# Optimization experiments

Hardware: AMD Instinct MI355X
Metric: run time of the kernel (lower is better)

## Reference

```python
import jax, jax.numpy as jnp
import numpy as np

N_NODES = 1_000_000
N_EDGES = 16_000_000


def setup_inputs() -> dict:
    key = jax.random.key(0)
    k1, k2, k3, k4 = jax.random.split(key, 4)
    x = jax.random.normal(k1, (N_NODES, 2), dtype=jnp.float32)
    edge_index = jax.random.randint(k2, (2, N_EDGES), 0, N_NODES, dtype=jnp.int64)
    W1 = jax.random.normal(k3, (2, 4), dtype=jnp.float32) * 0.5
    b1 = jnp.zeros((4,), dtype=jnp.float32)
    W2 = jax.random.normal(k4, (4, 2), dtype=jnp.float32) * 0.5
    b2 = jnp.zeros((2,), dtype=jnp.float32)
    return {"x": x, "edge_index": edge_index, "W1": W1, "b1": b1, "W2": W2, "b2": b2}


def _gcn_conv(h, src, dst, norm, b, n_nodes):
    # h already linearly transformed: message = h[src] * norm, scatter-add to dst
    msg = h[src] * norm[:, None]
    out = jax.ops.segment_sum(msg, dst, num_segments=n_nodes)
    return out + b


def reference(x, edge_index, W1, b1, W2, b2):
    n = x.shape[0]
    loop = jnp.arange(n, dtype=edge_index.dtype)
    # PyG GCNConv default: add self-loops, symmetric deg^{-1/2} normalization
    src = jnp.concatenate([edge_index[0], loop])
    dst = jnp.concatenate([edge_index[1], loop])
    deg = jax.ops.segment_sum(jnp.ones_like(src, dtype=x.dtype), dst, num_segments=n)
    dinv = jnp.where(deg > 0, jax.lax.rsqrt(deg), 0.0)
    norm = dinv[src] * dinv[dst]

    h = _gcn_conv(x @ W1, src, dst, norm, b1, n)   # conv1: [N,2] -> [N,4]
    h = jax.nn.relu(h)
    out = _gcn_conv(h @ W2, src, dst, norm, b2, n)  # conv2: [N,4] -> [N,2]
    return out
```

## Files before the change

kernel.cpp:

```cpp
#include <hip/hip_runtime.h>
#include <hip/hip_fp16.h>


constexpr int W_SHIFT = 11;
constexpr int W = 2048;
constexpr int MAXB = 512;
constexpr int RB = 1024;
constexpr int CHUNK = 8192;
constexpr int CAP = 28;
constexpr int AB = 512;

constexpr float SCALE1 = 65536.0f;
constexpr float INV1   = 1.0f / 65536.0f;
constexpr unsigned BIAS1 = 1u << 20;
constexpr float SCALE2 = 4096.0f;
constexpr float INV2   = 1.0f / 4096.0f;
constexpr unsigned BIAS2 = 1u << 22;

typedef unsigned uv4 __attribute__((ext_vector_type(4)));
typedef int      iv4 __attribute__((ext_vector_type(4)));

__device__ __forceinline__ unsigned long long pack2(float a, float b,
                                                    float scale, unsigned bias) {
    unsigned lo = (unsigned)(__float2int_rn(a * scale) + (int)bias);
    unsigned hi = (unsigned)(__float2int_rn(b * scale) + (int)bias);
    return (unsigned long long)lo | ((unsigned long long)hi << 32);
}

__global__ __launch_bounds__(256) void k_zero_fill(unsigned* __restrict__ fill,
                                                   int nb, unsigned C) {
    int i = blockIdx.x * 256 + threadIdx.x;
    if (i < nb) fill[i] = (unsigned)i * C;
}

__global__ __launch_bounds__(RB) void k_reorder(const int* __restrict__ src,
                                                const int* __restrict__ dst,
                                                unsigned* __restrict__ fill,
                                                unsigned* __restrict__ perm, int E) {
    __shared__ unsigned slab[MAXB * CAP];
    __shared__ unsigned ptr[MAXB];
    __shared__ unsigned gbase[MAXB];
    int tid = threadIdx.x;
    if (tid < MAXB) ptr[tid] = 0u;
    __syncthreads();
    long base0 = (long)blockIdx.x * CHUNK;
    int total = (int)min((long)CHUNK, (long)E - base0);
    bool full = (total == CHUNK);

    if (full) {
        const iv4* dv4 = (const iv4*)(dst + base0);
        const iv4* sv4 = (const iv4*)(src + base0);
        #pragma unroll
        for (int k = 0; k < 2; k++) {
            iv4 dq = dv4[k * RB + tid];
            iv4 sq = sv4[k * RB + tid];
            unsigned d, b, val, lpos;
            d = (unsigned)dq.x; b = d >> W_SHIFT;
            val = (unsigned)sq.x | ((d & (W - 1)) << 20);
            lpos = atomicAdd(&ptr[b], 1u);
            if (lpos < (unsigned)CAP) slab[b * CAP + lpos] = val;
            else perm[atomicAdd(&fill[b], 1u)] = val;
            d = (unsigned)dq.y; b = d >> W_SHIFT;
            val = (unsigned)sq.y | ((d & (W - 1)) << 20);
            lpos = atomicAdd(&ptr[b], 1u);
            if (lpos < (unsigned)CAP) slab[b * CAP + lpos] = val;
            else perm[atomicAdd(&fill[b], 1u)] = val;
            d = (unsigned)dq.z; b = d >> W_SHIFT;
            val = (unsigned)sq.z | ((d & (W - 1)) << 20);
            lpos = atomicAdd(&ptr[b], 1u);
            if (lpos < (unsigned)CAP) slab[b * CAP + lpos] = val;
            else perm[atomicAdd(&fill[b], 1u)] = val;
            d = (unsigned)dq.w; b = d >> W_SHIFT;
            val = (unsigned)sq.w | ((d & (W - 1)) << 20);
            lpos = atomicAdd(&ptr[b], 1u);
            if (lpos < (unsigned)CAP) slab[b * CAP + lpos] = val;
            else perm[atomicAdd(&fill[b], 1u)] = val;
        }
    } else {
        for (int li = tid; li < total; li += RB) {
            unsigned d = (unsigned)dst[base0 + li];
            unsigned s = (unsigned)src[base0 + li];
            unsigned b = d >> W_SHIFT;
            unsigned val = s | ((d & (W - 1)) << 20);
            unsigned lpos = atomicAdd(&ptr[b], 1u);
            if (lpos < (unsigned)CAP) slab[b * CAP + lpos] = val;
            else perm[atomicAdd(&fill[b], 1u)] = val;
        }
    }
    __syncthreads();
    if (tid < MAXB) {
        unsigned cnt = min(ptr[tid], (unsigned)CAP);
        gbase[tid] = cnt ? atomicAdd(&fill[tid], cnt) : 0u;
        ptr[tid] = cnt;
    }
    __syncthreads();
    for (int s = tid; s < MAXB * CAP; s += RB) {
        int b = s / CAP;
        int i = s - b * CAP;
        if (i < (int)ptr[b]) perm[gbase[b] + i] = slab[s];
    }
}

__global__ __launch_bounds__(AB) void k_dinv(const unsigned* __restrict__ perm,
                                             const unsigned* __restrict__ fill,
                                             const float2* __restrict__ x,
                                             float* __restrict__ dinv,
                                             unsigned* __restrict__ deg,
                                             __half2* __restrict__ xs,
                                             int N, unsigned C) {
    __shared__ unsigned c[2 * W];
    for (int i = threadIdx.x; i < 2 * W; i += AB) c[i] = 0u;
    __syncthreads();
    int b = blockIdx.x;
    unsigned par = threadIdx.x & 1u;
    unsigned s = (unsigned)b * C, e = fill[b];
    unsigned m = e - s, nv8 = m >> 3;
    const uv4* p4 = (const uv4*)(perm + s);
    for (unsigned j = threadIdx.x; j < nv8; j += AB) {
        uv4 qa = __builtin_nontemporal_load(p4 + 2u * j);
        uv4 qb = __builtin_nontemporal_load(p4 + 2u * j + 1u);
        atomicAdd(&c[((qa.x >> 20) << 1) | par], 1u);
        atomicAdd(&c[((qa.y >> 20) << 1) | par], 1u);
        atomicAdd(&c[((qa.z >> 20) << 1) | par], 1u);
        atomicAdd(&c[((qa.w >> 20) << 1) | par], 1u);
        atomicAdd(&c[((qb.x >> 20) << 1) | par], 1u);
        atomicAdd(&c[((qb.y >> 20) << 1) | par], 1u);
        atomicAdd(&c[((qb.z >> 20) << 1) | par], 1u);
        atomicAdd(&c[((qb.w >> 20) << 1) | par], 1u);
    }
    unsigned t = s + (nv8 << 3) + threadIdx.x;
    if (t < e) atomicAdd(&c[((perm[t] >> 20) << 1) | par], 1u);
    __syncthreads();
    int d0 = b << W_SHIFT;
    for (int l = threadIdx.x; l < W; l += AB) {
        int d = d0 + l;
        if (d < N) {
            unsigned cn = c[2 * l] + c[2 * l + 1];
            float dv = 1.0f / sqrtf((float)(cn + 1u));
            dinv[d] = dv;
            deg[d] = cn;
            float2 xv = x[d];
            xs[d] = __floats2half2_rn(xv.x * dv, xv.y * dv);
        }
    }
}

__global__ __launch_bounds__(AB) void k_acc1(const unsigned* __restrict__ perm,
                                             const unsigned* __restrict__ fill,
                                             const __half2* __restrict__ xs,
                                             const float* __restrict__ dinv,
                                             const unsigned* __restrict__ deg,
                                             const float* __restrict__ W1,
                                             const float* __restrict__ b1,
                                             const float* __restrict__ W2,
                                             __half2* __restrict__ h2s,
                                             int N, unsigned C) {
    __shared__ unsigned long long acc[2 * W];
    for (int i = threadIdx.x; i < 2 * W; i += AB) acc[i] = 0ull;
    __syncthreads();
    int b = blockIdx.x;
    unsigned par = threadIdx.x & 1u;
    unsigned s = (unsigned)b * C, e = fill[b];
    unsigned m = e - s, nv8 = m >> 3;
    const uv4* p4 = (const uv4*)(perm + s);
    for (unsigned j = threadIdx.x; j < nv8; j += AB) {
        uv4 qa = __builtin_nontemporal_load(p4 + 2u * j);
        uv4 qb = __builtin_nontemporal_load(p4 + 2u * j + 1u);
        float2 v0 = __half22float2(xs[qa.x & 0xFFFFFu]);
        float2 v1 = __half22float2(xs[qa.y & 0xFFFFFu]);
        float2 v2 = __half22float2(xs[qa.z & 0xFFFFFu]);
        float2 v3 = __half22float2(xs[qa.w & 0xFFFFFu]);
        float2 v4 = __half22float2(xs[qb.x & 0xFFFFFu]);
        float2 v5 = __half22float2(xs[qb.y & 0xFFFFFu]);
        float2 v6 = __half22float2(xs[qb.z & 0xFFFFFu]);
        float2 v7 = __half22float2(xs[qb.w & 0xFFFFFu]);
        atomicAdd(&acc[((qa.x >> 20) << 1) | par], pack2(v0.x, v0.y, SCALE1, BIAS1));
        atomicAdd(&acc[((qa.y >> 20) << 1) | par], pack2(v1.x, v1.y, SCALE1, BIAS1));
        atomicAdd(&acc[((qa.z >> 20) << 1) | par], pack2(v2.x, v2.y, SCALE1, BIAS1));
        atomicAdd(&acc[((qa.w >> 20) << 1) | par], pack2(v3.x, v3.y, SCALE1, BIAS1));
        atomicAdd(&acc[((qb.x >> 20) << 1) | par], pack2(v4.x, v4.y, SCALE1, BIAS1));
        atomicAdd(&acc[((qb.y >> 20) << 1) | par], pack2(v5.x, v5.y, SCALE1, BIAS1));
        atomicAdd(&acc[((qb.z >> 20) << 1) | par], pack2(v6.x, v6.y, SCALE1, BIAS1));
        atomicAdd(&acc[((qb.w >> 20) << 1) | par], pack2(v7.x, v7.y, SCALE1, BIAS1));
    }
    unsigned t = s + (nv8 << 3) + threadIdx.x;
    if (t < e) {
        unsigned p = perm[t];
        float2 v = __half22float2(xs[p & 0xFFFFFu]);
        atomicAdd(&acc[((p >> 20) << 1) | par], pack2(v.x, v.y, SCALE1, BIAS1));
    }
    __syncthreads();
    int d0 = b << W_SHIFT;
    float w10 = W1[0], w11 = W1[1], w12 = W1[2], w13 = W1[3];
    float w14 = W1[4], w15 = W1[5], w16 = W1[6], w17 = W1[7];
    float bb0 = b1[0], bb1 = b1[1], bb2 = b1[2], bb3 = b1[3];
    float u0 = W2[0], u1 = W2[1], u2 = W2[2], u3 = W2[3];
    float u4 = W2[4], u5 = W2[5], u6 = W2[6], u7 = W2[7];
    for (int l = threadIdx.x; l < W; l += AB) {
        int d = d0 + l;
        if (d < N) {
            float dv = dinv[d];
            unsigned cn = deg[d];
            unsigned long long a64 = acc[2 * l] + acc[2 * l + 1];
            unsigned lo = (unsigned)a64, hi = (unsigned)(a64 >> 32);
            float2 self = __half22float2(xs[d]);
            float Sx = (float)(int)(lo - cn * BIAS1) * INV1 + self.x;
            float Sy = (float)(int)(hi - cn * BIAS1) * INV1 + self.y;
            float a0 = fmaxf(fmaf(Sy, w14, Sx * w10) * dv + bb0, 0.0f);
            float a1 = fmaxf(fmaf(Sy, w15, Sx * w11) * dv + bb1, 0.0f);
            float a2 = fmaxf(fmaf(Sy, w16, Sx * w12) * dv + bb2, 0.0f);
            float a3 = fmaxf(fmaf(Sy, w17, Sx * w13) * dv + bb3, 0.0f);
            float hx = (a0 * u0 + a1 * u2 + a2 * u4 + a3 * u6) * dv;
            float hy = (a0 * u1 + a1 * u3 + a2 * u5 + a3 * u7) * dv;
            h2s[d] = __floats2half2_rn(hx, hy);
        }
    }
}

__global__ __launch_bounds__(AB) void k_acc2(const unsigned* __restrict__ perm,
                                             const unsigned* __restrict__ fill,
                                             const __half2* __restrict__ h2s,
                                             const float* __restrict__ dinv,
                                             const unsigned* __restrict__ deg,
                                             const float* __restrict__ b2,
                                             float2* __restrict__ out,
                                             int N, unsigned C) {
    __shared__ unsigned long long acc[2 * W];
    for (int i = threadIdx.x; i < 2 * W; i += AB) acc[i] = 0ull;
    __syncthreads();
    int b = blockIdx.x;
    unsigned par = threadIdx.x & 1u;
    unsigned s = (unsigned)b * C, e = fill[b];
    unsigned m = e - s, nv8 = m >> 3;
    const uv4* p4 = (const uv4*)(perm + s);
    for (unsigned j = threadIdx.x; j < nv8; j += AB) {
        uv4 qa = __builtin_nontemporal_load(p4 + 2u * j);
        uv4 qb = __builtin_nontemporal_load(p4 + 2u * j + 1u);
        float2 v0 = __half22float2(h2s[qa.x & 0xFFFFFu]);
        float2 v1 = __half22float2(h2s[qa.y & 0xFFFFFu]);
        float2 v2 = __half22float2(h2s[qa.z & 0xFFFFFu]);
        float2 v3 = __half22float2(h2s[qa.w & 0xFFFFFu]);
        float2 v4 = __half22float2(h2s[qb.x & 0xFFFFFu]);
        float2 v5 = __half22float2(h2s[qb.y & 0xFFFFFu]);
        float2 v6 = __half22float2(h2s[qb.z & 0xFFFFFu]);
        float2 v7 = __half22float2(h2s[qb.w & 0xFFFFFu]);
        atomicAdd(&acc[((qa.x >> 20) << 1) | par], pack2(v0.x, v0.y, SCALE2, BIAS2));
        atomicAdd(&acc[((qa.y >> 20) << 1) | par], pack2(v1.x, v1.y, SCALE2, BIAS2));
        atomicAdd(&acc[((qa.z >> 20) << 1) | par], pack2(v2.x, v2.y, SCALE2, BIAS2));
        atomicAdd(&acc[((qa.w >> 20) << 1) | par], pack2(v3.x, v3.y, SCALE2, BIAS2));
        atomicAdd(&acc[((qb.x >> 20) << 1) | par], pack2(v4.x, v4.y, SCALE2, BIAS2));
        atomicAdd(&acc[((qb.y >> 20) << 1) | par], pack2(v5.x, v5.y, SCALE2, BIAS2));
        atomicAdd(&acc[((qb.z >> 20) << 1) | par], pack2(v6.x, v6.y, SCALE2, BIAS2));
        atomicAdd(&acc[((qb.w >> 20) << 1) | par], pack2(v7.x, v7.y, SCALE2, BIAS2));
    }
    unsigned t = s + (nv8 << 3) + threadIdx.x;
    if (t < e) {
        unsigned p = perm[t];
        float2 v = __half22float2(h2s[p & 0xFFFFFu]);
        atomicAdd(&acc[((p >> 20) << 1) | par], pack2(v.x, v.y, SCALE2, BIAS2));
    }
    __syncthreads();
    int d0 = b << W_SHIFT;
    float bb0 = b2[0], bb1 = b2[1];
    for (int l = threadIdx.x; l < W; l += AB) {
        int d = d0 + l;
        if (d < N) {
            float dv = dinv[d];
            unsigned cn = deg[d];
            unsigned long long a64 = acc[2 * l] + acc[2 * l + 1];
            unsigned lo = (unsigned)a64, hi = (unsigned)(a64 >> 32);
            float2 v = __half22float2(h2s[d]);
            float Sx = (float)(int)(lo - cn * BIAS2) * INV2 + v.x;
            float Sy = (float)(int)(hi - cn * BIAS2) * INV2 + v.y;
            out[d] = make_float2(Sx * dv + bb0, Sy * dv + bb1);
        }
    }
}


__global__ __launch_bounds__(256) void f_init_deg(unsigned* deg, int n) {
    int i = blockIdx.x * 256 + threadIdx.x;
    if (i < n) deg[i] = 1u;
}
__global__ __launch_bounds__(256) void f_count_deg(const int* dst, unsigned* deg, int E) {
    int e = blockIdx.x * 256 + threadIdx.x;
    if (e < E) atomicAdd(&deg[dst[e]], 1u);
}
__global__ __launch_bounds__(256) void f_node1(const float2* x, const float* W1,
                                               const unsigned* deg, float* dinv,
                                               float4* h1s, float4* agg1, int n) {
    int i = blockIdx.x * 256 + threadIdx.x;
    if (i >= n) return;
    float dv = 1.0f / sqrtf((float)deg[i]);
    dinv[i] = dv;
    float2 xv = x[i];
    float4 h;
    h.x = fmaf(xv.y, W1[4], xv.x * W1[0]) * dv;
    h.y = fmaf(xv.y, W1[5], xv.x * W1[1]) * dv;
    h.z = fmaf(xv.y, W1[6], xv.x * W1[2]) * dv;
    h.w = fmaf(xv.y, W1[7], xv.x * W1[3]) * dv;
    h1s[i] = h;
    agg1[i] = make_float4(h.x * dv, h.y * dv, h.z * dv, h.w * dv);
}
__global__ __launch_bounds__(256) void f_edge1(const int* src, const int* dst,
                                               const float* dinv, const float4* h1s,
                                               float* agg1, int E) {
    int e = blockIdx.x * 256 + threadIdx.x;
    if (e >= E) return;
    int s = src[e], d = dst[e];
    float w = dinv[d];
    float4 m = h1s[s];
    float* p = agg1 + 4ll * d;
    unsafeAtomicAdd(p + 0, m.x * w);
    unsafeAtomicAdd(p + 1, m.y * w);
    unsafeAtomicAdd(p + 2, m.z * w);
    unsafeAtomicAdd(p + 3, m.w * w);
}
__global__ __launch_bounds__(256) void f_node2(const float4* agg1, const float* b1,
                                               const float* W2, const float* b2,
                                               const float* dinv, float2* h2s,
                                               float2* out, int n) {
    int i = blockIdx.x * 256 + threadIdx.x;
    if (i >= n) return;
    float4 a = agg1[i];
    a.x = fmaxf(a.x + b1[0], 0.0f);
    a.y = fmaxf(a.y + b1[1], 0.0f);
    a.z = fmaxf(a.z + b1[2], 0.0f);
    a.w = fmaxf(a.w + b1[3], 0.0f);
    float dv = dinv[i];
    float2 h;
    h.x = (a.x * W2[0] + a.y * W2[2] + a.z * W2[4] + a.w * W2[6]) * dv;
    h.y = (a.x * W2[1] + a.y * W2[3] + a.z * W2[5] + a.w * W2[7]) * dv;
    h2s[i] = h;
    out[i] = make_float2(b2[0] + h.x * dv, b2[1] + h.y * dv);
}
__global__ __launch_bounds__(256) void f_edge2(const int* src, const int* dst,
                                               const float* dinv, const float2* h2s,
                                               float* out, int E) {
    int e = blockIdx.x * 256 + threadIdx.x;
    if (e >= E) return;
    int s = src[e], d = dst[e];
    float w = dinv[d];
    float2 m = h2s[s];
    float* p = out + 2ll * d;
    unsafeAtomicAdd(p + 0, m.x * w);
    unsafeAtomicAdd(p + 1, m.y * w);
}

extern "C" void kernel_launch(void* const* d_in, const int* in_sizes, int n_in,
                              void* d_out, int out_size, void* d_ws, size_t ws_size,
                              hipStream_t stream) {
    const float* x  = (const float*)d_in[0];
    const int* ei   = (const int*)d_in[1];
    const float* W1 = (const float*)d_in[2];
    const float* b1 = (const float*)d_in[3];
    const float* W2 = (const float*)d_in[4];
    const float* b2 = (const float*)d_in[5];
    float* out = (float*)d_out;

    const int N = in_sizes[0] / 2;
    const int E = in_sizes[1] / 2;
    const int* src = ei;
    const int* dst = ei + E;
    const int NB = (N + W - 1) >> W_SHIFT;

    char* ws = (char*)d_ws;
    const int gN = (N + 255) / 256;
    const int gE = (E + 255) / 256;

    size_t fixed = 32768 + (size_t)16 * N;
    long avail = (long)ws_size - (long)fixed;
    long Cmax = (avail > 0) ? avail / (4L * NB) : 0;
    long Cmin = (long)(E / (NB > 0 ? NB : 1)) + 4096;
    long Cw = (Cmax > Cmin + 8192) ? (Cmin + 8192) : Cmax;
    unsigned C = (unsigned)(Cw & ~7L);
    bool fast = ((long)C >= Cmin) && (NB <= MAXB) && (N <= (1 << 20));

    if (fast) {
        unsigned* fill = (unsigned*)(ws);
        float*    dinv = (float*)(ws + 32768);
        unsigned* deg  = (unsigned*)(ws + 32768 + (size_t)4 * N);
        __half2*  xs   = (__half2*)(ws + 32768 + (size_t)8 * N);
        __half2*  h2s  = (__half2*)(ws + 32768 + (size_t)12 * N);
        unsigned* perm = (unsigned*)(ws + fixed);

        k_zero_fill<<<(NB + 255) / 256, 256, 0, stream>>>(fill, NB, C);
        k_reorder<<<(E + CHUNK - 1) / CHUNK, RB, 0, stream>>>(src, dst, fill, perm, E);
        k_dinv<<<NB, AB, 0, stream>>>(perm, fill, (const float2*)x, dinv, deg, xs, N, C);
        k_acc1<<<NB, AB, 0, stream>>>(perm, fill, xs, dinv, deg, W1, b1, W2, h2s, N, C);
        k_acc2<<<NB, AB, 0, stream>>>(perm, fill, h2s, dinv, deg, b2, (float2*)out, N, C);
    } else {
        unsigned* deg = (unsigned*)(ws);
        float* dinv   = (float*)(ws + (size_t)4 * N);
        float* h1s    = (float*)(ws + (size_t)8 * N);
        float* agg1   = (float*)(ws + (size_t)24 * N);
        float* h2s    = h1s;

        f_init_deg<<<gN, 256, 0, stream>>>(deg, N);
        f_count_deg<<<gE, 256, 0, stream>>>(dst, deg, E);
        f_node1<<<gN, 256, 0, stream>>>((const float2*)x, W1, deg, dinv,
                                        (float4*)h1s, (float4*)agg1, N);
        f_edge1<<<gE, 256, 0, stream>>>(src, dst, dinv, (const float4*)h1s, agg1, E);
        f_node2<<<gN, 256, 0, stream>>>((const float4*)agg1, b1, W2, b2, dinv,
                                        (float2*)h2s, (float2*)out, N);
        f_edge2<<<gE, 256, 0, stream>>>(src, dst, dinv, (const float2*)h2s, out, E);
    }
}
```

Measured before the change: 431.3 us.

## Build per-destination CSR within windows and use gather-based accumulation

Adds a second-level sort that turns each destination window's bucketed edges into a full CSR (offsets plus source list). Degrees and dinv are computed from the counts in the same pass. The two aggregation passes become pull-style gathers per destination node with register accumulation, replacing the shared-memory atomic scatter over each window. The cost is an extra read and write of the edge list plus more workspace, and the per-thread loops can be imbalanced when degrees vary.

```diff
diff --git a/kernel.cpp b/kernel.cpp
--- a/kernel.cpp
+++ b/kernel.cpp
@@ -101,6 +101,205 @@
     }
 }
 
+__global__ __launch_bounds__(AB) void k_sortwin(const unsigned* __restrict__ perm,
+                                                const unsigned* __restrict__ fill,
+                                                const float2* __restrict__ x,
+                                                __half2* __restrict__ xs,
+                                                unsigned* __restrict__ offs,
+                                                unsigned* __restrict__ perm2,
+                                                int N, unsigned C, int NB) {
+    __shared__ unsigned cnt[2 * W];
+    __shared__ unsigned scn[AB];
+    __shared__ unsigned sh_base, sh_tot;
+    const int tid = threadIdx.x;
+    const int b = blockIdx.x;
+
+    unsigned wsz = (tid < NB) ? (fill[tid] - (unsigned)tid * C) : 0u;
+    scn[tid] = wsz;
+    __syncthreads();
+    for (int off = 1; off < AB; off <<= 1) {
+        unsigned u = (tid >= off) ? scn[tid - off] : 0u;
+        __syncthreads();
+        scn[tid] += u;
+        __syncthreads();
+    }
+    if (tid == 0) {
+        sh_base = (b > 0) ? scn[b - 1] : 0u;
+        sh_tot  = scn[AB - 1];
+    }
+    for (int i = tid; i < 2 * W; i += AB) cnt[i] = 0u;
+    __syncthreads();
+
+    unsigned s = (unsigned)b * C, e = fill[b];
+    unsigned m = e - s, nv8 = m >> 3;
+    unsigned par = tid & 1u;
+    const uv4* p4 = (const uv4*)(perm + s);
+    for (unsigned j = tid; j < nv8; j += AB) {
+        uv4 qa = __builtin_nontemporal_load(p4 + 2u * j);
+        uv4 qb = __builtin_nontemporal_load(p4 + 2u * j + 1u);
+        atomicAdd(&cnt[((qa.x >> 20) << 1) | par], 1u);
+        atomicAdd(&cnt[((qa.y >> 20) << 1) | par], 1u);
+        atomicAdd(&cnt[((qa.z >> 20) << 1) | par], 1u);
+        atomicAdd(&cnt[((qa.w >> 20) << 1) | par], 1u);
+        atomicAdd(&cnt[((qb.x >> 20) << 1) | par], 1u);
+        atomicAdd(&cnt[((qb.y >> 20) << 1) | par], 1u);
+        atomicAdd(&cnt[((qb.z >> 20) << 1) | par], 1u);
+        atomicAdd(&cnt[((qb.w >> 20) << 1) | par], 1u);
+    }
+    unsigned t8 = s + (nv8 << 3) + (unsigned)tid;
+    if (t8 < e) atomicAdd(&cnt[((perm[t8] >> 20) << 1) | par], 1u);
+    __syncthreads();
+
+    int l0 = 4 * tid;
+    unsigned c0 = cnt[2 * l0]     + cnt[2 * l0 + 1];
+    unsigned c1 = cnt[2 * l0 + 2] + cnt[2 * l0 + 3];
+    unsigned c2 = cnt[2 * l0 + 4] + cnt[2 * l0 + 5];
+    unsigned c3 = cnt[2 * l0 + 6] + cnt[2 * l0 + 7];
+    unsigned sum4 = c0 + c1 + c2 + c3;
+    scn[tid] = sum4;
+    __syncthreads();
+    for (int off = 1; off < AB; off <<= 1) {
+        unsigned u = (tid >= off) ? scn[tid - off] : 0u;
+        __syncthreads();
+        scn[tid] += u;
+        __syncthreads();
+    }
+    unsigned base = sh_base + (scn[tid] - sum4);
+    unsigned o0 = base, o1 = o0 + c0, o2 = o1 + c1, o3 = o2 + c2;
+    cnt[l0] = o0; cnt[l0 + 1] = o1; cnt[l0 + 2] = o2; cnt[l0 + 3] = o3;
+
+    int d0 = (b << W_SHIFT) + l0;
+    if (d0     <= N) offs[d0]     = o0;
+    if (d0 + 1 <= N) offs[d0 + 1] = o1;
+    if (d0 + 2 <= N) offs[d0 + 2] = o2;
+    if (d0 + 3 <= N) offs[d0 + 3] = o3;
+    if (b == 0 && tid == 0) offs[N] = sh_tot;
+
+    unsigned cc[4] = {c0, c1, c2, c3};
+    #pragma unroll
+    for (int k = 0; k < 4; k++) {
+        int d = d0 + k;
+        if (d < N) {
+            float dv = 1.0f / sqrtf((float)cc[k] + 1.0f);
+            float2 xv = x[d];
+            xs[d] = __floats2half2_rn(xv.x * dv, xv.y * dv);
+        }
+    }
+    __syncthreads();
+
+    for (unsigned j = tid; j < nv8; j += AB) {
+        uv4 qa = __builtin_nontemporal_load(p4 + 2u * j);
+        uv4 qb = __builtin_nontemporal_load(p4 + 2u * j + 1u);
+        unsigned p;
+        p = atomicAdd(&cnt[qa.x >> 20], 1u); perm2[p] = qa.x & 0xFFFFFu;
+        p = atomicAdd(&cnt[qa.y >> 20], 1u); perm2[p] = qa.y & 0xFFFFFu;
+        p = atomicAdd(&cnt[qa.z >> 20], 1u); perm2[p] = qa.z & 0xFFFFFu;
+        p = atomicAdd(&cnt[qa.w >> 20], 1u); perm2[p] = qa.w & 0xFFFFFu;
+        p = atomicAdd(&cnt[qb.x >> 20], 1u); perm2[p] = qb.x & 0xFFFFFu;
+        p = atomicAdd(&cnt[qb.y >> 20], 1u); perm2[p] = qb.y & 0xFFFFFu;
+        p = atomicAdd(&cnt[qb.z >> 20], 1u); perm2[p] = qb.z & 0xFFFFFu;
+        p = atomicAdd(&cnt[qb.w >> 20], 1u); perm2[p] = qb.w & 0xFFFFFu;
+    }
+    if (t8 < e) {
+        unsigned v = perm[t8];
+        unsigned p = atomicAdd(&cnt[v >> 20], 1u);
+        perm2[p] = v & 0xFFFFFu;
+    }
+}
+
+__global__ __launch_bounds__(AB) void k_gacc1(const unsigned* __restrict__ perm2,
+                                              const unsigned* __restrict__ offs,
+                                              const __half2* __restrict__ xs,
+                                              const float* __restrict__ W1,
+                                              const float* __restrict__ b1,
+                                              const float* __restrict__ W2,
+                                              __half2* __restrict__ h2s, int N) {
+    int d0 = (blockIdx.x << W_SHIFT) + 4 * (int)threadIdx.x;
+    if (d0 >= N) return;
+    uv4 ov = *(const uv4*)(offs + d0);
+    unsigned o4 = offs[d0 + 4];
+    float w10 = W1[0], w11 = W1[1], w12 = W1[2], w13 = W1[3];
+    float w14 = W1[4], w15 = W1[5], w16 = W1[6], w17 = W1[7];
+    float bb0 = b1[0], bb1 = b1[1], bb2 = b1[2], bb3 = b1[3];
+    float u0 = W2[0], u1 = W2[1], u2 = W2[2], u3 = W2[3];
+    float u4 = W2[4], u5 = W2[5], u6 = W2[6], u7 = W2[7];
+    unsigned stA[4] = {ov.x, ov.y, ov.z, ov.w};
+    unsigned enA[4] = {ov.y, ov.z, ov.w, o4};
+    #pragma unroll
+    for (int k = 0; k < 4; k++) {
+        int d = d0 + k;
+        if (d < N) {
+            unsigned st = stA[k], en = enA[k];
+            float dv = 1.0f / sqrtf((float)(en - st) + 1.0f);
+            float2 self = __half22float2(xs[d]);
+            float Sx = self.x, Sy = self.y;
+            unsigned i = st;
+            for (; i + 4 <= en; i += 4) {
+                unsigned s0 = perm2[i], s1 = perm2[i + 1];
+                unsigned s2 = perm2[i + 2], s3 = perm2[i + 3];
+                float2 v0 = __half22float2(xs[s0]);
+                float2 v1 = __half22float2(xs[s1]);
+                float2 v2 = __half22float2(xs[s2]);
+                float2 v3 = __half22float2(xs[s3]);
+                Sx += (v0.x + v1.x) + (v2.x + v3.x);
+                Sy += (v0.y + v1.y) + (v2.y + v3.y);
+            }
+            for (; i < en; i++) {
+                float2 v = __half22float2(xs[perm2[i]]);
+                Sx += v.x; Sy += v.y;
+            }
+            float a0 = fmaxf(fmaf(Sy, w14, Sx * w10) * dv + bb0, 0.0f);
+            float a1 = fmaxf(fmaf(Sy, w15, Sx * w11) * dv + bb1, 0.0f);
+            float a2 = fmaxf(fmaf(Sy, w16, Sx * w12) * dv + bb2, 0.0f);
+            float a3 = fmaxf(fmaf(Sy, w17, Sx * w13) * dv + bb3, 0.0f);
+            float hx = (a0 * u0 + a1 * u2 + a2 * u4 + a3 * u6) * dv;
+            float hy = (a0 * u1 + a1 * u3 + a2 * u5 + a3 * u7) * dv;
+            h2s[d] = __floats2half2_rn(hx, hy);
+        }
+    }
+}
+
+__global__ __launch_bounds__(AB) void k_gacc2(const unsigned* __restrict__ perm2,
+                                              const unsigned* __restrict__ offs,
+                                              const __half2* __restrict__ h2s,
+                                              const float* __restrict__ b2,
+                                              float2* __restrict__ out, int N) {
+    int d0 = (blockIdx.x << W_SHIFT) + 4 * (int)threadIdx.x;
+    if (d0 >= N) return;
+    uv4 ov = *(const uv4*)(offs + d0);
+    unsigned o4 = offs[d0 + 4];
+    float bb0 = b2[0], bb1 = b2[1];
+    unsigned stA[4] = {ov.x, ov.y, ov.z, ov.w};
+    unsigned enA[4] = {ov.y, ov.z, ov.w, o4};
+    #pragma unroll
+    for (int k = 0; k < 4; k++) {
+        int d = d0 + k;
+        if (d < N) {
+            unsigned st = stA[k], en = enA[k];
+            float dv = 1.0f / sqrtf((float)(en - st) + 1.0f);
+            float2 self = __half22float2(h2s[d]);
+            float Sx = self.x, Sy = self.y;
+            unsigned i = st;
+            for (; i + 4 <= en; i += 4) {
+                unsigned s0 = perm2[i], s1 = perm2[i + 1];
+                unsigned s2 = perm2[i + 2], s3 = perm2[i + 3];
+                float2 v0 = __half22float2(h2s[s0]);
+                float2 v1 = __half22float2(h2s[s1]);
+                float2 v2 = __half22float2(h2s[s2]);
+                float2 v3 = __half22float2(h2s[s3]);
+                Sx += (v0.x + v1.x) + (v2.x + v3.x);
+                Sy += (v0.y + v1.y) + (v2.y + v3.y);
+            }
+            for (; i < en; i++) {
+                float2 v = __half22float2(h2s[perm2[i]]);
+                Sx += v.x; Sy += v.y;
+            }
+            out[d] = make_float2(Sx * dv + bb0, Sy * dv + bb1);
+        }
+    }
+}
+
+
 __global__ __launch_bounds__(AB) void k_dinv(const unsigned* __restrict__ perm,
                                              const unsigned* __restrict__ fill,
                                              const float2* __restrict__ x,
@@ -368,15 +567,41 @@
     const int gN = (N + 255) / 256;
     const int gE = (E + 255) / 256;
 
+    const long Cmin = (long)(E / (NB > 0 ? NB : 1)) + 4096;
+    auto rnd = [](size_t v) { return (v + 63) & ~(size_t)63; };
+
+    size_t sz_xs   = rnd((size_t)4 * N);
+    size_t sz_offs = rnd((size_t)4 * (N + 16));
+    size_t sz_p2   = rnd((size_t)4 * (size_t)E);
+    size_t fixed2  = 32768 + sz_xs + sz_xs + sz_offs + sz_p2 + 64;
+    long avail2 = (long)ws_size - (long)fixed2;
+    long Cmax2 = (avail2 > 0) ? avail2 / (4L * NB) : 0;
+    long Cw2 = (Cmax2 > Cmin + 8192) ? (Cmin + 8192) : Cmax2;
+    unsigned C2 = (unsigned)(Cw2 & ~7L);
+    bool fast2 = ((long)C2 >= Cmin) && (NB <= MAXB) && (N <= (1 << 20)) && (E > 0);
+
     size_t fixed = 32768 + (size_t)16 * N;
     long avail = (long)ws_size - (long)fixed;
     long Cmax = (avail > 0) ? avail / (4L * NB) : 0;
-    long Cmin = (long)(E / (NB > 0 ? NB : 1)) + 4096;
     long Cw = (Cmax > Cmin + 8192) ? (Cmin + 8192) : Cmax;
     unsigned C = (unsigned)(Cw & ~7L);
     bool fast = ((long)C >= Cmin) && (NB <= MAXB) && (N <= (1 << 20));
 
-    if (fast) {
+    if (fast2) {
+        unsigned* fill  = (unsigned*)ws;
+        __half2*  xs    = (__half2*)(ws + 32768);
+        __half2*  h2s   = (__half2*)(ws + 32768 + sz_xs);
+        unsigned* offs  = (unsigned*)(ws + 32768 + 2 * sz_xs);
+        unsigned* perm2 = (unsigned*)(ws + 32768 + 2 * sz_xs + sz_offs);
+        unsigned* perm  = (unsigned*)(ws + 32768 + 2 * sz_xs + sz_offs + sz_p2);
+
+        k_zero_fill<<<(NB + 255) / 256, 256, 0, stream>>>(fill, NB, C2);
+        k_reorder<<<(E + CHUNK - 1) / CHUNK, RB, 0, stream>>>(src, dst, fill, perm, E);
+        k_sortwin<<<NB, AB, 0, stream>>>(perm, fill, (const float2*)x, xs, offs,
+                                         perm2, N, C2, NB);
+        k_gacc1<<<NB, AB, 0, stream>>>(perm2, offs, xs, W1, b1, W2, h2s, N);
+        k_gacc2<<<NB, AB, 0, stream>>>(perm2, offs, h2s, b2, (float2*)out, N);
+    } else if (fast) {
         unsigned* fill = (unsigned*)(ws);
         float*    dinv = (float*)(ws + 32768);
         unsigned* deg  = (unsigned*)(ws + 32768 + (size_t)4 * N);
```

New measurement: 810.4 us. 87.9% more time.

## Fuse reorder, degree and both aggregation stages into one cooperative kernel

Applied to the files above, without the earlier changes.

Replaces the five separate launches (fill init, edge reorder, degree/dinv, conv1, conv2) with a single cooperative kernel. Stages are separated by grid-wide syncs, and one shared-memory union holds the slab, count and accumulator buffers. The reorder stage becomes a grid-stride loop over chunks run by NB blocks of 512 threads. The goal is to remove per-launch gaps and the separate dinv buffer. The cost is far fewer resident waves during the reorder stage, plus grid-sync overhead.

```diff
diff --git a/kernel.cpp b/kernel.cpp
--- a/kernel.cpp
+++ b/kernel.cpp
@@ -1,5 +1,8 @@
 #include <hip/hip_runtime.h>
 #include <hip/hip_fp16.h>
+#include <hip/hip_cooperative_groups.h>
+
+namespace cg = cooperative_groups;
 
 
 constexpr int W_SHIFT = 11;
@@ -8,6 +11,7 @@
 constexpr int RB = 1024;
 constexpr int CHUNK = 8192;
 constexpr int CAP = 28;
+constexpr int CT = 512;
 constexpr int AB = 512;
 
 constexpr float SCALE1 = 65536.0f;
@@ -26,6 +30,246 @@
     unsigned hi = (unsigned)(__float2int_rn(b * scale) + (int)bias);
     return (unsigned long long)lo | ((unsigned long long)hi << 32);
 }
+
+
+__global__ __launch_bounds__(CT, 4) void k_fused(
+    const int* __restrict__ src, const int* __restrict__ dst,
+    const float2* __restrict__ x,
+    const float* __restrict__ W1, const float* __restrict__ b1,
+    const float* __restrict__ W2, const float* __restrict__ b2,
+    unsigned* __restrict__ fill, unsigned* __restrict__ deg,
+    __half2* __restrict__ xs, __half2* __restrict__ h2s,
+    float2* __restrict__ out, unsigned* __restrict__ perm,
+    int N, int E, unsigned C, int NB, int NCH)
+{
+    __shared__ union ShU {
+        struct { unsigned slab[MAXB * CAP]; unsigned ptr[MAXB]; unsigned gbase[MAXB]; } r;
+        unsigned cnt[2 * W];
+        unsigned long long acc[2 * W];
+    } sh;
+    cg::grid_group grid = cg::this_grid();
+    const int tid = threadIdx.x;
+    const int bid = blockIdx.x;
+    const int b = bid;
+
+    if (bid == 0 && tid < NB) fill[tid] = (unsigned)tid * C;
+    grid.sync();
+
+    for (int cid = bid; cid < NCH; cid += gridDim.x) {
+        if (tid < MAXB) sh.r.ptr[tid] = 0u;
+        __syncthreads();
+        long base0 = (long)cid * CHUNK;
+        int total = (int)min((long)CHUNK, (long)E - base0);
+        bool full = (total == CHUNK);
+        if (full) {
+            const iv4* dv4 = (const iv4*)(dst + base0);
+            const iv4* sv4 = (const iv4*)(src + base0);
+            #pragma unroll
+            for (int k = 0; k < CHUNK / (4 * CT); k++) {
+                iv4 dq = dv4[k * CT + tid];
+                iv4 sq = sv4[k * CT + tid];
+                unsigned d, bb, val, lpos;
+                d = (unsigned)dq.x; bb = d >> W_SHIFT;
+                val = (unsigned)sq.x | ((d & (W - 1)) << 20);
+                lpos = atomicAdd(&sh.r.ptr[bb], 1u);
+                if (lpos < (unsigned)CAP) sh.r.slab[bb * CAP + lpos] = val;
+                else perm[atomicAdd(&fill[bb], 1u)] = val;
+                d = (unsigned)dq.y; bb = d >> W_SHIFT;
+                val = (unsigned)sq.y | ((d & (W - 1)) << 20);
+                lpos = atomicAdd(&sh.r.ptr[bb], 1u);
+                if (lpos < (unsigned)CAP) sh.r.slab[bb * CAP + lpos] = val;
+                else perm[atomicAdd(&fill[bb], 1u)] = val;
+                d = (unsigned)dq.z; bb = d >> W_SHIFT;
+                val = (unsigned)sq.z | ((d & (W - 1)) << 20);
+                lpos = atomicAdd(&sh.r.ptr[bb], 1u);
+                if (lpos < (unsigned)CAP) sh.r.slab[bb * CAP + lpos] = val;
+                else perm[atomicAdd(&fill[bb], 1u)] = val;
+                d = (unsigned)dq.w; bb = d >> W_SHIFT;
+                val = (unsigned)sq.w | ((d & (W - 1)) << 20);
+                lpos = atomicAdd(&sh.r.ptr[bb], 1u);
+                if (lpos < (unsigned)CAP) sh.r.slab[bb * CAP + lpos] = val;
+                else perm[atomicAdd(&fill[bb], 1u)] = val;
+            }
+        } else {
+            for (int li = tid; li < total; li += CT) {
+                unsigned d = (unsigned)dst[base0 + li];
+                unsigned s = (unsigned)src[base0 + li];
+                unsigned bb = d >> W_SHIFT;
+                unsigned val = s | ((d & (W - 1)) << 20);
+                unsigned lpos = atomicAdd(&sh.r.ptr[bb], 1u);
+                if (lpos < (unsigned)CAP) sh.r.slab[bb * CAP + lpos] = val;
+                else perm[atomicAdd(&fill[bb], 1u)] = val;
+            }
+        }
+        __syncthreads();
+        if (tid < MAXB) {
+            unsigned cnt = min(sh.r.ptr[tid], (unsigned)CAP);
+            sh.r.gbase[tid] = cnt ? atomicAdd(&fill[tid], cnt) : 0u;
+            sh.r.ptr[tid] = cnt;
+        }
+        __syncthreads();
+        for (int s2 = tid; s2 < MAXB * CAP; s2 += CT) {
+            int b2 = s2 / CAP;
+            int i2 = s2 - b2 * CAP;
+            if (i2 < (int)sh.r.ptr[b2]) perm[sh.r.gbase[b2] + i2] = sh.r.slab[s2];
+        }
+        __syncthreads();
+    }
+    __threadfence();
+    grid.sync();
+
+    {
+        for (int i = tid; i < 2 * W; i += CT) sh.cnt[i] = 0u;
+        __syncthreads();
+        unsigned par = tid & 1u;
+        unsigned s = (unsigned)b * C, e = fill[b];
+        unsigned m = e - s, nv8 = m >> 3;
+        const uv4* p4 = (const uv4*)(perm + s);
+        for (unsigned j = tid; j < nv8; j += CT) {
+            uv4 qa = __builtin_nontemporal_load(p4 + 2u * j);
+            uv4 qb = __builtin_nontemporal_load(p4 + 2u * j + 1u);
+            atomicAdd(&sh.cnt[((qa.x >> 20) << 1) | par], 1u);
+            atomicAdd(&sh.cnt[((qa.y >> 20) << 1) | par], 1u);
+            atomicAdd(&sh.cnt[((qa.z >> 20) << 1) | par], 1u);
+            atomicAdd(&sh.cnt[((qa.w >> 20) << 1) | par], 1u);
+            atomicAdd(&sh.cnt[((qb.x >> 20) << 1) | par], 1u);
+            atomicAdd(&sh.cnt[((qb.y >> 20) << 1) | par], 1u);
+            atomicAdd(&sh.cnt[((qb.z >> 20) << 1) | par], 1u);
+            atomicAdd(&sh.cnt[((qb.w >> 20) << 1) | par], 1u);
+        }
+        unsigned t = s + (nv8 << 3) + (unsigned)tid;
+        if (t < e) atomicAdd(&sh.cnt[((perm[t] >> 20) << 1) | par], 1u);
+        __syncthreads();
+        int d0 = b << W_SHIFT;
+        for (int l = tid; l < W; l += CT) {
+            int d = d0 + l;
+            if (d < N) {
+                unsigned cn = sh.cnt[2 * l] + sh.cnt[2 * l + 1];
+                float dv = 1.0f / sqrtf((float)(cn + 1u));
+                deg[d] = cn;
+                float2 xv = x[d];
+                xs[d] = __floats2half2_rn(xv.x * dv, xv.y * dv);
+            }
+        }
+    }
+    __threadfence();
+    grid.sync();
+
+    {
+        for (int i = tid; i < 2 * W; i += CT) sh.acc[i] = 0ull;
+        __syncthreads();
+        unsigned par = tid & 1u;
+        unsigned s = (unsigned)b * C, e = fill[b];
+        unsigned m = e - s, nv8 = m >> 3;
+        const uv4* p4 = (const uv4*)(perm + s);
+        for (unsigned j = tid; j < nv8; j += CT) {
+            uv4 qa = __builtin_nontemporal_load(p4 + 2u * j);
+            uv4 qb = __builtin_nontemporal_load(p4 + 2u * j + 1u);
+            float2 v0 = __half22float2(xs[qa.x & 0xFFFFFu]);
+            float2 v1 = __half22float2(xs[qa.y & 0xFFFFFu]);
+            float2 v2 = __half22float2(xs[qa.z & 0xFFFFFu]);
+            float2 v3 = __half22float2(xs[qa.w & 0xFFFFFu]);
+            float2 v4 = __half22float2(xs[qb.x & 0xFFFFFu]);
+            float2 v5 = __half22float2(xs[qb.y & 0xFFFFFu]);
+            float2 v6 = __half22float2(xs[qb.z & 0xFFFFFu]);
+            float2 v7 = __half22float2(xs[qb.w & 0xFFFFFu]);
+            atomicAdd(&sh.acc[((qa.x >> 20) << 1) | par], pack2(v0.x, v0.y, SCALE1, BIAS1));
+            atomicAdd(&sh.acc[((qa.y >> 20) << 1) | par], pack2(v1.x, v1.y, SCALE1, BIAS1));
+            atomicAdd(&sh.acc[((qa.z >> 20) << 1) | par], pack2(v2.x, v2.y, SCALE1, BIAS1));
+            atomicAdd(&sh.acc[((qa.w >> 20) << 1) | par], pack2(v3.x, v3.y, SCALE1, BIAS1));
+            atomicAdd(&sh.acc[((qb.x >> 20) << 1) | par], pack2(v4.x, v4.y, SCALE1, BIAS1));
+            atomicAdd(&sh.acc[((qb.y >> 20) << 1) | par], pack2(v5.x, v5.y, SCALE1, BIAS1));
+            atomicAdd(&sh.acc[((qb.z >> 20) << 1) | par], pack2(v6.x, v6.y, SCALE1, BIAS1));
+            atomicAdd(&sh.acc[((qb.w >> 20) << 1) | par], pack2(v7.x, v7.y, SCALE1, BIAS1));
+        }
+        unsigned t = s + (nv8 << 3) + (unsigned)tid;
+        if (t < e) {
+            unsigned p = perm[t];
+            float2 v = __half22float2(xs[p & 0xFFFFFu]);
+            atomicAdd(&sh.acc[((p >> 20) << 1) | par], pack2(v.x, v.y, SCALE1, BIAS1));
+        }
+        __syncthreads();
+        int d0 = b << W_SHIFT;
+        float w10 = W1[0], w11 = W1[1], w12 = W1[2], w13 = W1[3];
+        float w14 = W1[4], w15 = W1[5], w16 = W1[6], w17 = W1[7];
+        float bb0 = b1[0], bb1 = b1[1], bb2 = b1[2], bb3 = b1[3];
+        float u0 = W2[0], u1 = W2[1], u2 = W2[2], u3 = W2[3];
+        float u4 = W2[4], u5 = W2[5], u6 = W2[6], u7 = W2[7];
+        for (int l = tid; l < W; l += CT) {
+            int d = d0 + l;
+            if (d < N) {
+                unsigned cn = deg[d];
+                float dv = 1.0f / sqrtf((float)(cn + 1u));
+                unsigned long long a64 = sh.acc[2 * l] + sh.acc[2 * l + 1];
+                unsigned lo = (unsigned)a64, hi = (unsigned)(a64 >> 32);
+                float2 self = __half22float2(xs[d]);
+                float Sx = (float)(int)(lo - cn * BIAS1) * INV1 + self.x;
+                float Sy = (float)(int)(hi - cn * BIAS1) * INV1 + self.y;
+                float a0 = fmaxf(fmaf(Sy, w14, Sx * w10) * dv + bb0, 0.0f);
+                float a1 = fmaxf(fmaf(Sy, w15, Sx * w11) * dv + bb1, 0.0f);
+                float a2 = fmaxf(fmaf(Sy, w16, Sx * w12) * dv + bb2, 0.0f);
+                float a3 = fmaxf(fmaf(Sy, w17, Sx * w13) * dv + bb3, 0.0f);
+                float hx = (a0 * u0 + a1 * u2 + a2 * u4 + a3 * u6) * dv;
+                float hy = (a0 * u1 + a1 * u3 + a2 * u5 + a3 * u7) * dv;
+                h2s[d] = __floats2half2_rn(hx, hy);
+            }
+        }
+    }
+    __threadfence();
+    grid.sync();
+
+    {
+        for (int i = tid; i < 2 * W; i += CT) sh.acc[i] = 0ull;
+        __syncthreads();
+        unsigned par = tid & 1u;
+        unsigned s = (unsigned)b * C, e = fill[b];
+        unsigned m = e - s, nv8 = m >> 3;
+        const uv4* p4 = (const uv4*)(perm + s);
+        for (unsigned j = tid; j < nv8; j += CT) {
+            uv4 qa = __builtin_nontemporal_load(p4 + 2u * j);
+            uv4 qb = __builtin_nontemporal_load(p4 + 2u * j + 1u);
+            float2 v0 = __half22float2(h2s[qa.x & 0xFFFFFu]);
+            float2 v1 = __half22float2(h2s[qa.y & 0xFFFFFu]);
+            float2 v2 = __half22float2(h2s[qa.z & 0xFFFFFu]);
+            float2 v3 = __half22float2(h2s[qa.w & 0xFFFFFu]);
+            float2 v4 = __half22float2(h2s[qb.x & 0xFFFFFu]);
+            float2 v5 = __half22float2(h2s[qb.y & 0xFFFFFu]);
+            float2 v6 = __half22float2(h2s[qb.z & 0xFFFFFu]);
+            float2 v7 = __half22float2(h2s[qb.w & 0xFFFFFu]);
+            atomicAdd(&sh.acc[((qa.x >> 20) << 1) | par], pack2(v0.x, v0.y, SCALE2, BIAS2));
+            atomicAdd(&sh.acc[((qa.y >> 20) << 1) | par], pack2(v1.x, v1.y, SCALE2, BIAS2));
+            atomicAdd(&sh.acc[((qa.z >> 20) << 1) | par], pack2(v2.x, v2.y, SCALE2, BIAS2));
+            atomicAdd(&sh.acc[((qa.w >> 20) << 1) | par], pack2(v3.x, v3.y, SCALE2, BIAS2));
+            atomicAdd(&sh.acc[((qb.x >> 20) << 1) | par], pack2(v4.x, v4.y, SCALE2, BIAS2));
+            atomicAdd(&sh.acc[((qb.y >> 20) << 1) | par], pack2(v5.x, v5.y, SCALE2, BIAS2));
+            atomicAdd(&sh.acc[((qb.z >> 20) << 1) | par], pack2(v6.x, v6.y, SCALE2, BIAS2));
+            atomicAdd(&sh.acc[((qb.w >> 20) << 1) | par], pack2(v7.x, v7.y, SCALE2, BIAS2));
+        }
+        unsigned t = s + (nv8 << 3) + (unsigned)tid;
+        if (t < e) {
+            unsigned p = perm[t];
+            float2 v = __half22float2(h2s[p & 0xFFFFFu]);
+            atomicAdd(&sh.acc[((p >> 20) << 1) | par], pack2(v.x, v.y, SCALE2, BIAS2));
+        }
+        __syncthreads();
+        int d0 = b << W_SHIFT;
+        float bb0 = b2[0], bb1 = b2[1];
+        for (int l = tid; l < W; l += CT) {
+            int d = d0 + l;
+            if (d < N) {
+                unsigned cn = deg[d];
+                float dv = 1.0f / sqrtf((float)(cn + 1u));
+                unsigned long long a64 = sh.acc[2 * l] + sh.acc[2 * l + 1];
+                unsigned lo = (unsigned)a64, hi = (unsigned)(a64 >> 32);
+                float2 v = __half22float2(h2s[d]);
+                float Sx = (float)(int)(lo - cn * BIAS2) * INV2 + v.x;
+                float Sy = (float)(int)(hi - cn * BIAS2) * INV2 + v.y;
+                out[d] = make_float2(Sx * dv + bb0, Sy * dv + bb1);
+            }
+        }
+    }
+}
+
 
 __global__ __launch_bounds__(256) void k_zero_fill(unsigned* __restrict__ fill,
                                                    int nb, unsigned C) {
@@ -46,7 +290,6 @@
     long base0 = (long)blockIdx.x * CHUNK;
     int total = (int)min((long)CHUNK, (long)E - base0);
     bool full = (total == CHUNK);
-
     if (full) {
         const iv4* dv4 = (const iv4*)(dst + base0);
         const iv4* sv4 = (const iv4*)(src + base0);
@@ -54,37 +297,37 @@
         for (int k = 0; k < 2; k++) {
             iv4 dq = dv4[k * RB + tid];
             iv4 sq = sv4[k * RB + tid];
-            unsigned d, b, val, lpos;
-            d = (unsigned)dq.x; b = d >> W_SHIFT;
+            unsigned d, bb, val, lpos;
+            d = (unsigned)dq.x; bb = d >> W_SHIFT;
             val = (unsigned)sq.x | ((d & (W - 1)) << 20);
-            lpos = atomicAdd(&ptr[b], 1u);
-            if (lpos < (unsigned)CAP) slab[b * CAP + lpos] = val;
-            else perm[atomicAdd(&fill[b], 1u)] = val;
-            d = (unsigned)dq.y; b = d >> W_SHIFT;
+            lpos = atomicAdd(&ptr[bb], 1u);
+            if (lpos < (unsigned)CAP) slab[bb * CAP + lpos] = val;
+            else perm[atomicAdd(&fill[bb], 1u)] = val;
+            d = (unsigned)dq.y; bb = d >> W_SHIFT;
             val = (unsigned)sq.y | ((d & (W - 1)) << 20);
-            lpos = atomicAdd(&ptr[b], 1u);
-            if (lpos < (unsigned)CAP) slab[b * CAP + lpos] = val;
-            else perm[atomicAdd(&fill[b], 1u)] = val;
-            d = (unsigned)dq.z; b = d >> W_SHIFT;
+            lpos = atomicAdd(&ptr[bb], 1u);
+            if (lpos < (unsigned)CAP) slab[bb * CAP + lpos] = val;
+            else perm[atomicAdd(&fill[bb], 1u)] = val;
+            d = (unsigned)dq.z; bb = d >> W_SHIFT;
             val = (unsigned)sq.z | ((d & (W - 1)) << 20);
-            lpos = atomicAdd(&ptr[b], 1u);
-            if (lpos < (unsigned)CAP) slab[b * CAP + lpos] = val;
-            else perm[atomicAdd(&fill[b], 1u)] = val;
-            d = (unsigned)dq.w; b = d >> W_SHIFT;
+            lpos = atomicAdd(&ptr[bb], 1u);
+            if (lpos < (unsigned)CAP) slab[bb * CAP + lpos] = val;
+            else perm[atomicAdd(&fill[bb], 1u)] = val;
+            d = (unsigned)dq.w; bb = d >> W_SHIFT;
             val = (unsigned)sq.w | ((d & (W - 1)) << 20);
-            lpos = atomicAdd(&ptr[b], 1u);
-            if (lpos < (unsigned)CAP) slab[b * CAP + lpos] = val;
-            else perm[atomicAdd(&fill[b], 1u)] = val;
+            lpos = atomicAdd(&ptr[bb], 1u);
+            if (lpos < (unsigned)CAP) slab[bb * CAP + lpos] = val;
+            else perm[atomicAdd(&fill[bb], 1u)] = val;
         }
     } else {
         for (int li = tid; li < total; li += RB) {
             unsigned d = (unsigned)dst[base0 + li];
             unsigned s = (unsigned)src[base0 + li];
-            unsigned b = d >> W_SHIFT;
+            unsigned bb = d >> W_SHIFT;
             unsigned val = s | ((d & (W - 1)) << 20);
-            unsigned lpos = atomicAdd(&ptr[b], 1u);
-            if (lpos < (unsigned)CAP) slab[b * CAP + lpos] = val;
-            else perm[atomicAdd(&fill[b], 1u)] = val;
+            unsigned lpos = atomicAdd(&ptr[bb], 1u);
+            if (lpos < (unsigned)CAP) slab[bb * CAP + lpos] = val;
+            else perm[atomicAdd(&fill[bb], 1u)] = val;
         }
     }
     __syncthreads();
@@ -95,9 +338,9 @@
     }
     __syncthreads();
     for (int s = tid; s < MAXB * CAP; s += RB) {
-        int b = s / CAP;
-        int i = s - b * CAP;
-        if (i < (int)ptr[b]) perm[gbase[b] + i] = slab[s];
+        int bb = s / CAP;
+        int i = s - bb * CAP;
+        if (i < (int)ptr[bb]) perm[gbase[bb] + i] = slab[s];
     }
 }
 
@@ -363,20 +606,47 @@
     const int* src = ei;
     const int* dst = ei + E;
     const int NB = (N + W - 1) >> W_SHIFT;
+    const int NCH = (E + CHUNK - 1) / CHUNK;
 
     char* ws = (char*)d_ws;
     const int gN = (N + 255) / 256;
     const int gE = (E + 255) / 256;
+    const long Cmin = (long)(E / (NB > 0 ? NB : 1)) + 4096;
+
+    size_t fixedc = 32768 + (size_t)12 * N;
+    long availc = (long)ws_size - (long)fixedc;
+    long Cmaxc = (availc > 0) ? availc / (4L * NB) : 0;
+    long Cwc = (Cmaxc > Cmin + 8192) ? (Cmin + 8192) : Cmaxc;
+    unsigned Cc = (unsigned)(Cwc & ~7L);
+    bool coop = ((long)Cc >= Cmin) && (NB <= MAXB) && (N <= (1 << 20)) && (E > 0);
 
     size_t fixed = 32768 + (size_t)16 * N;
     long avail = (long)ws_size - (long)fixed;
     long Cmax = (avail > 0) ? avail / (4L * NB) : 0;
-    long Cmin = (long)(E / (NB > 0 ? NB : 1)) + 4096;
     long Cw = (Cmax > Cmin + 8192) ? (Cmin + 8192) : Cmax;
     unsigned C = (unsigned)(Cw & ~7L);
     bool fast = ((long)C >= Cmin) && (NB <= MAXB) && (N <= (1 << 20));
 
-    if (fast) {
+    if (coop) {
+        unsigned* fill = (unsigned*)ws;
+        unsigned* deg  = (unsigned*)(ws + 32768);
+        __half2*  xs   = (__half2*)(ws + 32768 + (size_t)4 * N);
+        __half2*  h2s  = (__half2*)(ws + 32768 + (size_t)8 * N);
+        unsigned* perm = (unsigned*)(ws + fixedc);
+        const float2* xp = (const float2*)x;
+        float2* outp = (float2*)out;
+        int Nv = N, Ev = E, NBv = NB, NCHv = NCH;
+        unsigned Cv = Cc;
+        void* args[] = {
+            (void*)&src, (void*)&dst, (void*)&xp,
+            (void*)&W1, (void*)&b1, (void*)&W2, (void*)&b2,
+            (void*)&fill, (void*)&deg, (void*)&xs, (void*)&h2s,
+            (void*)&outp, (void*)&perm,
+            (void*)&Nv, (void*)&Ev, (void*)&Cv, (void*)&NBv, (void*)&NCHv
+        };
+        hipLaunchCooperativeKernel((const void*)k_fused, dim3(NB), dim3(CT),
+                                   args, 0u, stream);
+    } else if (fast) {
         unsigned* fill = (unsigned*)(ws);
         float*    dinv = (float*)(ws + 32768);
         unsigned* deg  = (unsigned*)(ws + 32768 + (size_t)4 * N);
```

New measurement: 998.9 us. 132% more time.
